# Kernel tuning notes

Hardware: AMD Instinct MI355X
Metric: run time of the kernel (lower is better)

The kernel has to match this reference:

```python
import jax, jax.numpy as jnp
import numpy as np

B, S, HID = 2, 2048, 2048
H = 16
Q_LORA, KV_LORA = 1536, 512
D_NOPE, D_ROPE, D_V = 128, 64, 128
D_QK = D_NOPE + D_ROPE  # 192
EPS = 1e-6


def rms_norm(x, w):
    var = jnp.mean(jnp.square(x), axis=-1, keepdims=True)
    return x * jax.lax.rsqrt(var + EPS) * w


def apply_rope(x, cos, sin):
    # x: [..., d] with interleaved (real, imag) pairs; cos/sin broadcastable to [..., d//2]
    xr = x[..., 0::2]
    xi = x[..., 1::2]
    or_ = xr * cos - xi * sin
    oi_ = xr * sin + xi * cos
    return jnp.stack([or_, oi_], axis=-1).reshape(x.shape)


def setup_inputs() -> dict:
    key = jax.random.key(0)
    ks = jax.random.split(key, 8)
    std = 0.02
    x = jax.random.normal(ks[0], (B, S, HID), dtype=jnp.float32)
    # rotary frequencies (real cos/sin pair per complex freq)
    inv_freq = 1.0 / (10000.0 ** (np.arange(0, D_ROPE, 2, dtype=np.float32) / D_ROPE))
    t = np.arange(S, dtype=np.float32)
    ang = np.outer(t, inv_freq)  # [S, D_ROPE//2]
    freqs_cis = jnp.asarray(np.stack([np.cos(ang), np.sin(ang)], axis=-1))  # [S, 32, 2]
    return {
        "x": x,
        "freqs_cis": freqs_cis,
        "wq_a": std * jax.random.normal(ks[1], (Q_LORA, HID), dtype=jnp.float32),
        "q_a_norm_w": jnp.ones((Q_LORA,), dtype=jnp.float32),
        "wq_b": std * jax.random.normal(ks[2], (H * D_QK, Q_LORA), dtype=jnp.float32),
        "wkv_a": std * jax.random.normal(ks[3], (KV_LORA + D_ROPE, HID), dtype=jnp.float32),
        "kv_norm_w": jnp.ones((KV_LORA,), dtype=jnp.float32),
        "wkv_b": std * jax.random.normal(ks[4], (H * (D_NOPE + D_V), KV_LORA), dtype=jnp.float32),
        "wo": std * jax.random.normal(ks[5], (HID, H * D_V), dtype=jnp.float32),
    }


def mla_forward(x, freqs_cis, wq_a, q_a_norm_w, wq_b, wkv_a, kv_norm_w, wkv_b, wo):
    cos = freqs_cis[..., 0]  # [S, D_ROPE//2]
    sin = freqs_cis[..., 1]
    # --- queries: low-rank down, RMSNorm, up ---
    q = rms_norm(x @ wq_a.T, q_a_norm_w) @ wq_b.T          # [B,S,H*D_QK]
    q = q.reshape(B, S, H, D_QK)
    q_nope, q_pe = q[..., :D_NOPE], q[..., D_NOPE:]
    q_pe = apply_rope(q_pe, cos[None, :, None, :], sin[None, :, None, :])
    q = jnp.concatenate([q_nope, q_pe], axis=-1)           # [B,S,H,D_QK]
    # --- kv latent + shared rope key ---
    kv_all = x @ wkv_a.T                                   # [B,S,KV_LORA+D_ROPE]
    kv_lat, k_pe = kv_all[..., :KV_LORA], kv_all[..., KV_LORA:]
    k_pe = apply_rope(k_pe, cos[None, :, :], sin[None, :, :])   # [B,S,D_ROPE]
    kv = rms_norm(kv_lat, kv_norm_w) @ wkv_b.T             # [B,S,H*(D_NOPE+D_V)]
    kv = kv.reshape(B, S, H, D_NOPE + D_V)
    k_nope, v = kv[..., :D_NOPE], kv[..., D_NOPE:]
    k = jnp.concatenate(
        [k_nope, jnp.broadcast_to(k_pe[:, :, None, :], (B, S, H, D_ROPE))], axis=-1
    )                                                      # [B,S,H,D_QK]
    # --- causal softmax attention ---
    scale = D_QK ** -0.5
    scores = jnp.einsum("bqhd,bkhd->bhqk", q, k) * scale   # [B,H,S,S]
    causal = jnp.tril(jnp.ones((S, S), dtype=bool))
    scores = jnp.where(causal, scores, jnp.finfo(scores.dtype).min)
    probs = jax.nn.softmax(scores, axis=-1)
    out = jnp.einsum("bhqk,bkhd->bqhd", probs, v)          # [B,S,H,D_V]
    return out.reshape(B, S, H * D_V) @ wo.T               # [B,S,HID]


def reference(x, freqs_cis, wq_a, q_a_norm_w, wq_b, wkv_a, kv_norm_w, wkv_b, wo):
    return mla_forward(x, freqs_cis, wq_a, q_a_norm_w, wq_b, wkv_a, kv_norm_w, wkv_b, wo)
```

## Files before the change

kernel.cpp:

```cpp
#include <hip/hip_runtime.h>

typedef __bf16 bf16_t;
typedef bf16_t bf16x8 __attribute__((ext_vector_type(8)));
typedef bf16_t bf16x4v __attribute__((ext_vector_type(4)));
typedef float f32x4 __attribute__((ext_vector_type(4)));

static constexpr float QSCALE = 0.07216878364870323f * 1.44269504088896341f;

#define AS1 __attribute__((address_space(1)))
#define AS3 __attribute__((address_space(3)))
__device__ __forceinline__ void g2lds16(const void* g, void* l) {
  __builtin_amdgcn_global_load_lds((const AS1 void*)g, (AS3 void*)l, 16, 0, 0);
}

__global__ void k_cast_bf16(const float* __restrict__ in, bf16_t* __restrict__ out, int n8) {
  int i = blockIdx.x * 256 + threadIdx.x;
  if (i >= n8) return;
  const float4* p = (const float4*)in + (size_t)i * 2;
  float4 a = p[0], b = p[1];
  bf16x8 o = {(bf16_t)a.x, (bf16_t)a.y, (bf16_t)a.z, (bf16_t)a.w,
              (bf16_t)b.x, (bf16_t)b.y, (bf16_t)b.z, (bf16_t)b.w};
  ((bf16x8*)out)[i] = o;
}

__global__ __launch_bounds__(256) void k_gemm(
    const bf16_t* __restrict__ A, const bf16_t* __restrict__ Bt,
    float* __restrict__ C, int M, int N, int K) {
  __shared__ __align__(16) bf16_t As[128][32];
  __shared__ __align__(16) bf16_t Bs[128][32];
  const int tid = threadIdx.x;
  const int lane = tid & 63, wid = tid >> 6;
  const int wr = wid >> 1, wc = wid & 1;
  const int lr = lane & 15, lk = lane >> 4;
  const int bm = blockIdx.y * 128, bn = blockIdx.x * 128;
  f32x4 acc[4][4] = {};
  const int srow = wid * 16 + (lane >> 2);
  const int scol = (lane & 3) * 8;
  const bf16_t* a0 = A + (size_t)(bm + srow) * K + scol;
  const bf16_t* a1 = A + (size_t)(bm + 64 + srow) * K + scol;
  const bf16_t* b0 = Bt + (size_t)(bn + srow) * K + scol;
  const bf16_t* b1 = Bt + (size_t)(bn + 64 + srow) * K + scol;
  bf16_t* lA0 = &As[wid * 16][0];
  bf16_t* lA1 = &As[64 + wid * 16][0];
  bf16_t* lB0 = &Bs[wid * 16][0];
  bf16_t* lB1 = &Bs[64 + wid * 16][0];
  for (int kt = 0; kt < K; kt += 32) {
    g2lds16(a0 + kt, lA0);
    g2lds16(a1 + kt, lA1);
    g2lds16(b0 + kt, lB0);
    g2lds16(b1 + kt, lB1);
    __syncthreads();
    bf16x8 af[4], bff[4];
#pragma unroll
    for (int i = 0; i < 4; i++)
      af[i] = *(const bf16x8*)(&As[wr * 64 + i * 16 + lr][lk * 8]);
#pragma unroll
    for (int j = 0; j < 4; j++)
      bff[j] = *(const bf16x8*)(&Bs[wc * 64 + j * 16 + lr][lk * 8]);
#pragma unroll
    for (int i = 0; i < 4; i++)
#pragma unroll
      for (int j = 0; j < 4; j++)
        acc[i][j] = __builtin_amdgcn_mfma_f32_16x16x32_bf16(af[i], bff[j], acc[i][j], 0, 0, 0);
    __syncthreads();
  }
  const int crow = bm + wr * 64 + lk * 4;
  const int ccol = bn + wc * 64 + lr;
#pragma unroll
  for (int i = 0; i < 4; i++)
#pragma unroll
    for (int j = 0; j < 4; j++) {
      int col = ccol + j * 16;
      if (col < N) {
#pragma unroll
        for (int r = 0; r < 4; r++)
          C[(size_t)(crow + i * 16 + r) * N + col] = acc[i][j][r];
      }
    }
}

__global__ __launch_bounds__(256) void k_rms_q(const float* __restrict__ in,
                                               const float* __restrict__ w,
                                               bf16_t* __restrict__ out) {
  int row = blockIdx.x;
  const float4* x4 = (const float4*)(in + (size_t)row * 1536);
  float ss = 0.f;
  for (int i = threadIdx.x; i < 384; i += 256) {
    float4 v = x4[i];
    ss += v.x * v.x + v.y * v.y + v.z * v.z + v.w * v.w;
  }
  for (int m = 32; m; m >>= 1) ss += __shfl_xor(ss, m);
  __shared__ float parts[4];
  if ((threadIdx.x & 63) == 0) parts[threadIdx.x >> 6] = ss;
  __syncthreads();
  float inv = rsqrtf((parts[0] + parts[1] + parts[2] + parts[3]) * (1.f / 1536.f) + 1e-6f);
  const float4* w4 = (const float4*)w;
  for (int i = threadIdx.x; i < 384; i += 256) {
    float4 v = x4[i];
    float4 ww = w4[i];
    bf16x4v o = {(bf16_t)(v.x * inv * ww.x), (bf16_t)(v.y * inv * ww.y),
                 (bf16_t)(v.z * inv * ww.z), (bf16_t)(v.w * inv * ww.w)};
    *(bf16x4v*)(out + (size_t)row * 1536 + i * 4) = o;
  }
}

__global__ __launch_bounds__(256) void k_kv_norm_rope(const float* __restrict__ kvall,
                                                      const float* __restrict__ w,
                                                      const float* __restrict__ freqs,
                                                      bf16_t* __restrict__ kvn,
                                                      bf16_t* __restrict__ Kf) {
  int row = blockIdx.x, tid = threadIdx.x;
  int b = row >> 11, s = row & 2047;
  const float* x = kvall + (size_t)row * 576;
  float ss = 0.f;
  float4 v = {0.f, 0.f, 0.f, 0.f};
  if (tid < 128) {
    v = ((const float4*)x)[tid];
    ss = v.x * v.x + v.y * v.y + v.z * v.z + v.w * v.w;
  }
  for (int m = 32; m; m >>= 1) ss += __shfl_xor(ss, m);
  __shared__ float parts[4];
  if ((tid & 63) == 0) parts[tid >> 6] = ss;
  __syncthreads();
  float inv = rsqrtf((parts[0] + parts[1] + parts[2] + parts[3]) * (1.f / 512.f) + 1e-6f);
  if (tid < 128) {
    float4 ww = ((const float4*)w)[tid];
    bf16x4v o = {(bf16_t)(v.x * inv * ww.x), (bf16_t)(v.y * inv * ww.y),
                 (bf16_t)(v.z * inv * ww.z), (bf16_t)(v.w * inv * ww.w)};
    *(bf16x4v*)(kvn + (size_t)row * 512 + tid * 4) = o;
  }
  if (tid < 32) {
    float xr = x[512 + 2 * tid], xi = x[513 + 2 * tid];
    float c = freqs[s * 64 + 2 * tid], sn = freqs[s * 64 + 2 * tid + 1];
    bf16_t o0 = (bf16_t)(xr * c - xi * sn);
    bf16_t o1 = (bf16_t)(xr * sn + xi * c);
#pragma unroll
    for (int h = 0; h < 16; h++) {
      size_t base = ((size_t)(b * 16 + h) * 2048 + s) * 192 + 128 + 2 * tid;
      Kf[base] = o0;
      Kf[base + 1] = o1;
    }
  }
}

__global__ __launch_bounds__(256) void k_q_rope(const float* __restrict__ q,
                                                const float* __restrict__ freqs,
                                                bf16_t* __restrict__ Q) {
  int row = blockIdx.x;
  int b = row >> 11, s = row & 2047;
  const float* src = q + (size_t)row * 3072;
  const float* fr = freqs + s * 64;
#pragma unroll
  for (int i = 0; i < 12; i++) {
    int idx = i * 256 + threadIdx.x;
    int h = idx / 192, d = idx - h * 192;
    float val;
    if (d < 128) {
      val = src[h * 192 + d];
    } else {
      int p = (d - 128) >> 1;
      float xr = src[h * 192 + 128 + 2 * p], xi = src[h * 192 + 129 + 2 * p];
      float c = fr[2 * p], sn = fr[2 * p + 1];
      val = ((d & 1) == 0) ? (xr * c - xi * sn) : (xr * sn + xi * c);
    }
    Q[((size_t)(b * 16 + h) * 2048 + s) * 192 + d] = (bf16_t)(val * QSCALE);
  }
}

__global__ __launch_bounds__(256) void k_split_kv(const float* __restrict__ kvfull,
                                                  bf16_t* __restrict__ Kf,
                                                  bf16_t* __restrict__ Vt) {
  __shared__ bf16_t vt_l[128][66];
  int s0 = blockIdx.x * 64;
  int h = blockIdx.y;
#pragma unroll 4
  for (int i = 0; i < 32; i++) {
    int idx = i * 256 + threadIdx.x;
    int r = idx >> 7, d = idx & 127;
    int row = s0 + r;
    int b = row >> 11, s = row & 2047;
    const float* src = kvfull + (size_t)row * 4096 + h * 256;
    float kn = src[d], vv = src[128 + d];
    Kf[((size_t)(b * 16 + h) * 2048 + s) * 192 + d] = (bf16_t)kn;
    vt_l[d][r] = (bf16_t)vv;
  }
  __syncthreads();
#pragma unroll 4
  for (int i = 0; i < 32; i++) {
    int idx = i * 256 + threadIdx.x;
    int d = idx >> 6, ss = idx & 63;
    int row = s0 + ss;
    int b = row >> 11, s = row & 2047;
    Vt[((size_t)(b * 16 + h) * 128 + d) * 2048 + s] = vt_l[d][ss];
  }
}

__global__ __launch_bounds__(256) void k_attn(const bf16_t* __restrict__ Q,
                                              const bf16_t* __restrict__ Kf,
                                              const bf16_t* __restrict__ Vt,
                                              bf16_t* __restrict__ O) {
  __shared__ __align__(16) bf16_t Ks[3][64][64];
  __shared__ __align__(16) bf16_t Vs[128][64];
  __shared__ __align__(16) bf16_t P[4][16][72];
  const int tid = threadIdx.x;
  const int lane = tid & 63, wid = tid >> 6;
  const int lr = lane & 15, lk = lane >> 4;
  const int qt = (int)gridDim.x - 1 - (int)blockIdx.x;
  const int qb = qt * 64;
  const int qbw = qb + wid * 16;
  const int bh = blockIdx.y;
  const int b = bh >> 4, h = bh & 15;
  const bf16_t* Qb = Q + (size_t)bh * 2048 * 192;
  const bf16_t* Kb = Kf + (size_t)bh * 2048 * 192;
  const bf16_t* Vb = Vt + (size_t)bh * 128 * 2048;
  bf16x8 bq[6];
#pragma unroll
  for (int f = 0; f < 6; f++)
    bq[f] = *(const bf16x8*)(Qb + (size_t)(qbw + lr) * 192 + f * 32 + lk * 8);
  f32x4 acc[8] = {};
  float m_s = -1e30f, l_s = 0.f;
  const int q_mine = qbw + lr;
  const int srowb = tid >> 3;
  const int sc8 = tid & 7;
  auto stage = [&](int k0) {
#pragma unroll
    for (int p = 0; p < 3; p++)
#pragma unroll
      for (int hh2 = 0; hh2 < 2; hh2++) {
        int row = hh2 * 32 + srowb;
        g2lds16(Kb + (size_t)(k0 + row) * 192 + p * 64 + ((sc8 ^ (row & 7)) * 8),
                &Ks[p][row][sc8 * 8]);
      }
#pragma unroll
    for (int j = 0; j < 4; j++) {
      int d = j * 32 + srowb;
      g2lds16(Vb + (size_t)d * 2048 + k0 + ((sc8 ^ (d & 7)) * 8), &Vs[d][sc8 * 8]);
    }
  };
  const int nkt = qt + 1;
  stage(0);
  for (int kt = 0; kt < nkt; kt++) {
    const int k0 = kt * 64;
    __syncthreads();
    f32x4 sc[4];
#pragma unroll
    for (int hh = 0; hh < 4; hh++) {
      f32x4 a = {};
      const int row = hh * 16 + lr;
      const int sw = (row & 7);
#pragma unroll
      for (int f = 0; f < 6; f++) {
        const int cc = (f & 1) * 4 + lk;
        bf16x8 ak = *(const bf16x8*)(&Ks[f >> 1][row][(cc ^ sw) * 8]);
        a = __builtin_amdgcn_mfma_f32_16x16x32_bf16(ak, bq[f], a, 0, 0, 0);
      }
      sc[hh] = a;
    }
    if (k0 + 63 > qbw) {
#pragma unroll
      for (int hh = 0; hh < 4; hh++) {
        int key = k0 + hh * 16 + lk * 4;
#pragma unroll
        for (int r = 0; r < 4; r++)
          if (key + r > q_mine) sc[hh][r] = -1e30f;
      }
    }
    float t0 = fmaxf(fmaxf(sc[0][0], sc[0][1]), fmaxf(sc[0][2], sc[0][3]));
    float t1 = fmaxf(fmaxf(sc[1][0], sc[1][1]), fmaxf(sc[1][2], sc[1][3]));
    float t2 = fmaxf(fmaxf(sc[2][0], sc[2][1]), fmaxf(sc[2][2], sc[2][3]));
    float t3 = fmaxf(fmaxf(sc[3][0], sc[3][1]), fmaxf(sc[3][2], sc[3][3]));
    float tmax = fmaxf(fmaxf(t0, t1), fmaxf(t2, t3));
    tmax = fmaxf(tmax, __shfl_xor(tmax, 16));
    tmax = fmaxf(tmax, __shfl_xor(tmax, 32));
    float mn = fmaxf(m_s, tmax);
    float alpha = exp2f(m_s - mn);
    m_s = mn;
    float sm = 0.f;
#pragma unroll
    for (int hh = 0; hh < 4; hh++) {
#pragma unroll
      for (int r = 0; r < 4; r++) {
        float p = exp2f(sc[hh][r] - mn);
        sc[hh][r] = p;
        sm += p;
      }
    }
    sm += __shfl_xor(sm, 16);
    sm += __shfl_xor(sm, 32);
    l_s = l_s * alpha + sm;
#pragma unroll
    for (int hh = 0; hh < 4; hh++) {
      bf16x4v pv = {(bf16_t)sc[hh][0], (bf16_t)sc[hh][1], (bf16_t)sc[hh][2], (bf16_t)sc[hh][3]};
      *(bf16x4v*)(&P[wid][lr][hh * 16 + lk * 4]) = pv;
    }
    float ab[4];
#pragma unroll
    for (int r = 0; r < 4; r++) ab[r] = __shfl(alpha, lk * 4 + r);
#pragma unroll
    for (int j = 0; j < 8; j++)
#pragma unroll
      for (int r = 0; r < 4; r++) acc[j][r] *= ab[r];
#pragma unroll
    for (int s2 = 0; s2 < 2; s2++) {
      bf16x8 pa = *(const bf16x8*)(&P[wid][lr][s2 * 32 + lk * 8]);
#pragma unroll
      for (int j = 0; j < 8; j++) {
        const int d = j * 16 + lr;
        const int cc = s2 * 4 + lk;
        bf16x8 bv = *(const bf16x8*)(&Vs[d][(cc ^ (d & 7)) * 8]);
        acc[j] = __builtin_amdgcn_mfma_f32_16x16x32_bf16(pa, bv, acc[j], 0, 0, 0);
      }
    }
    __syncthreads();
    if (kt + 1 < nkt) stage(k0 + 64);
  }
  float linv = 1.f / l_s;
  float lb[4];
#pragma unroll
  for (int r = 0; r < 4; r++) lb[r] = __shfl(linv, lk * 4 + r);
  size_t orow = (size_t)b * 2048 + qbw + lk * 4;
#pragma unroll
  for (int j = 0; j < 8; j++)
#pragma unroll
    for (int r = 0; r < 4; r++)
      O[(orow + r) * 2048 + h * 128 + j * 16 + lr] = (bf16_t)(acc[j][r] * lb[r]);
}

extern "C" void kernel_launch(void* const* d_in, const int* in_sizes, int n_in,
                              void* d_out, int out_size, void* d_ws, size_t ws_size,
                              hipStream_t stream) {
  const float* x = (const float*)d_in[0];
  const float* freqs = (const float*)d_in[1];
  const float* wq_a = (const float*)d_in[2];
  const float* q_norm_w = (const float*)d_in[3];
  const float* wq_b = (const float*)d_in[4];
  const float* wkv_a = (const float*)d_in[5];
  const float* kv_norm_w = (const float*)d_in[6];
  const float* wkv_b = (const float*)d_in[7];
  const float* wo = (const float*)d_in[8];
  float* out = (float*)d_out;
  char* ws = (char*)d_ws;

  float* f32scr = (float*)(ws);
  bf16_t* xbf = (bf16_t*)(ws + 67108864);
  bf16_t* wqab = (bf16_t*)(ws + 83886080);
  bf16_t* wqbb = (bf16_t*)(ws + 90177536);
  bf16_t* wkvab = (bf16_t*)(ws + 99614720);
  bf16_t* wkvbb = (bf16_t*)(ws + 101974016);
  bf16_t* wob = (bf16_t*)(ws + 106168320);
  bf16_t* qan = (bf16_t*)(ws + 114556928);
  bf16_t* kvn = (bf16_t*)(ws + 127139840);
  bf16_t* Qb = (bf16_t*)(ws + 131334144);
  bf16_t* Kb = (bf16_t*)(ws + 156499968);
  bf16_t* Vtb = (bf16_t*)(ws + 181665792);
  bf16_t* aob = (bf16_t*)(ws + 198443008);
  (void)in_sizes; (void)n_in; (void)out_size; (void)ws_size;

  auto cast = [&](const float* src, bf16_t* dst, int n) {
    int n8 = n / 8;
    k_cast_bf16<<<(n8 + 255) / 256, 256, 0, stream>>>(src, dst, n8);
  };
  cast(x, xbf, 8388608);
  cast(wq_a, wqab, 3145728);
  cast(wq_b, wqbb, 4718592);
  cast(wkv_a, wkvab, 1179648);
  cast(wkv_b, wkvbb, 2097152);
  cast(wo, wob, 4194304);

  k_gemm<<<dim3(5, 32), 256, 0, stream>>>(xbf, wkvab, f32scr, 4096, 576, 2048);
  k_kv_norm_rope<<<4096, 256, 0, stream>>>(f32scr, kv_norm_w, freqs, kvn, Kb);
  k_gemm<<<dim3(32, 32), 256, 0, stream>>>(kvn, wkvbb, f32scr, 4096, 4096, 512);
  k_split_kv<<<dim3(64, 16), 256, 0, stream>>>(f32scr, Kb, Vtb);
  k_gemm<<<dim3(12, 32), 256, 0, stream>>>(xbf, wqab, f32scr, 4096, 1536, 2048);
  k_rms_q<<<4096, 256, 0, stream>>>(f32scr, q_norm_w, qan);
  k_gemm<<<dim3(24, 32), 256, 0, stream>>>(qan, wqbb, f32scr, 4096, 3072, 1536);
  k_q_rope<<<4096, 256, 0, stream>>>(f32scr, freqs, Qb);
  k_attn<<<dim3(32, 32), 256, 0, stream>>>(Qb, Kb, Vtb, aob);
  k_gemm<<<dim3(16, 32), 256, 0, stream>>>(aob, wob, out, 4096, 2048, 2048);
}
```

Before: 582.8 us.

## Emit bf16 GEMM outputs, fuse Q rope into GEMM, widen attention blocks

GEMM becomes a template that writes bf16 intermediates instead of fp32, and in one mode applies RoPE, the softmax scale and the head-major scatter directly in the epilogue, which removes the separate q_rope kernel. The downstream norm and split kernels read bf16, halving their intermediate traffic. The attention kernel now uses 512-thread blocks covering 128 queries. It replaces async global-to-LDS staging with register prefetch plus commit, and adds a rotation swizzle on the P buffer. Causally dead tiles are skipped per wave. Rounding the pre-norm intermediates to bf16 adds extra error.

```diff
diff --git a/kernel.cpp b/kernel.cpp
--- a/kernel.cpp
+++ b/kernel.cpp
@@ -23,9 +23,10 @@
   ((bf16x8*)out)[i] = o;
 }
 
-__global__ __launch_bounds__(256) void k_gemm(
+template <int MODE>
+__global__ __launch_bounds__(256) void k_gemm_t(
     const bf16_t* __restrict__ A, const bf16_t* __restrict__ Bt,
-    float* __restrict__ C, int M, int N, int K) {
+    void* __restrict__ Cout, int M, int N, int K, const float* __restrict__ freqs) {
   __shared__ __align__(16) bf16_t As[128][32];
   __shared__ __align__(16) bf16_t Bs[128][32];
   const int tid = threadIdx.x;
@@ -72,51 +73,83 @@
     for (int j = 0; j < 4; j++) {
       int col = ccol + j * 16;
       if (col < N) {
-#pragma unroll
-        for (int r = 0; r < 4; r++)
-          C[(size_t)(crow + i * 16 + r) * N + col] = acc[i][j][r];
+        if constexpr (MODE == 0) {
+          float* C = (float*)Cout;
+#pragma unroll
+          for (int r = 0; r < 4; r++)
+            C[(size_t)(crow + i * 16 + r) * N + col] = acc[i][j][r];
+        } else if constexpr (MODE == 1) {
+          bf16_t* C = (bf16_t*)Cout;
+#pragma unroll
+          for (int r = 0; r < 4; r++)
+            C[(size_t)(crow + i * 16 + r) * N + col] = (bf16_t)acc[i][j][r];
+        } else {
+          bf16_t* Qd = (bf16_t*)Cout;
+          int hcol = col / 192;
+          int dmod = col - hcol * 192;
+#pragma unroll
+          for (int r = 0; r < 4; r++) {
+            int row = crow + i * 16 + r;
+            int bb = row >> 11, s = row & 2047;
+            float v = acc[i][j][r];
+            float partner = __shfl_xor(v, 1);
+            if (dmod >= 128) {
+              int p = (dmod - 128) >> 1;
+              int pbase = ((lr & 1) == 0) ? (dmod - 128) : (dmod - 129);
+              p = pbase >> 1;
+              float c = freqs[s * 64 + 2 * p];
+              float sn = freqs[s * 64 + 2 * p + 1];
+              v = ((lr & 1) == 0) ? (v * c - partner * sn) : (partner * sn + v * c);
+            }
+            Qd[((size_t)(bb * 16 + hcol) * 2048 + s) * 192 + dmod] = (bf16_t)(v * QSCALE);
+          }
+        }
       }
     }
 }
 
-__global__ __launch_bounds__(256) void k_rms_q(const float* __restrict__ in,
+__global__ __launch_bounds__(256) void k_rms_q(const bf16_t* __restrict__ in,
                                                const float* __restrict__ w,
                                                bf16_t* __restrict__ out) {
-  int row = blockIdx.x;
-  const float4* x4 = (const float4*)(in + (size_t)row * 1536);
+  int row = blockIdx.x, tid = threadIdx.x;
+  const bf16x8* x8 = (const bf16x8*)(in + (size_t)row * 1536);
   float ss = 0.f;
-  for (int i = threadIdx.x; i < 384; i += 256) {
-    float4 v = x4[i];
-    ss += v.x * v.x + v.y * v.y + v.z * v.z + v.w * v.w;
+  bf16x8 v = {};
+  if (tid < 192) {
+    v = x8[tid];
+#pragma unroll
+    for (int j = 0; j < 8; j++) { float f = (float)v[j]; ss += f * f; }
   }
   for (int m = 32; m; m >>= 1) ss += __shfl_xor(ss, m);
   __shared__ float parts[4];
-  if ((threadIdx.x & 63) == 0) parts[threadIdx.x >> 6] = ss;
+  if ((tid & 63) == 0) parts[tid >> 6] = ss;
   __syncthreads();
   float inv = rsqrtf((parts[0] + parts[1] + parts[2] + parts[3]) * (1.f / 1536.f) + 1e-6f);
-  const float4* w4 = (const float4*)w;
-  for (int i = threadIdx.x; i < 384; i += 256) {
-    float4 v = x4[i];
-    float4 ww = w4[i];
-    bf16x4v o = {(bf16_t)(v.x * inv * ww.x), (bf16_t)(v.y * inv * ww.y),
-                 (bf16_t)(v.z * inv * ww.z), (bf16_t)(v.w * inv * ww.w)};
-    *(bf16x4v*)(out + (size_t)row * 1536 + i * 4) = o;
-  }
-}
-
-__global__ __launch_bounds__(256) void k_kv_norm_rope(const float* __restrict__ kvall,
+  if (tid < 192) {
+    const float4* w4 = (const float4*)(w + tid * 8);
+    float4 w0 = w4[0], w1 = w4[1];
+    bf16x8 o = {(bf16_t)((float)v[0] * inv * w0.x), (bf16_t)((float)v[1] * inv * w0.y),
+                (bf16_t)((float)v[2] * inv * w0.z), (bf16_t)((float)v[3] * inv * w0.w),
+                (bf16_t)((float)v[4] * inv * w1.x), (bf16_t)((float)v[5] * inv * w1.y),
+                (bf16_t)((float)v[6] * inv * w1.z), (bf16_t)((float)v[7] * inv * w1.w)};
+    *(bf16x8*)(out + (size_t)row * 1536 + tid * 8) = o;
+  }
+}
+
+__global__ __launch_bounds__(256) void k_kv_norm_rope(const bf16_t* __restrict__ kvall,
                                                       const float* __restrict__ w,
                                                       const float* __restrict__ freqs,
                                                       bf16_t* __restrict__ kvn,
                                                       bf16_t* __restrict__ Kf) {
   int row = blockIdx.x, tid = threadIdx.x;
   int b = row >> 11, s = row & 2047;
-  const float* x = kvall + (size_t)row * 576;
+  const bf16_t* x = kvall + (size_t)row * 576;
   float ss = 0.f;
-  float4 v = {0.f, 0.f, 0.f, 0.f};
+  float vf[4] = {0.f, 0.f, 0.f, 0.f};
   if (tid < 128) {
-    v = ((const float4*)x)[tid];
-    ss = v.x * v.x + v.y * v.y + v.z * v.z + v.w * v.w;
+    bf16x4v v4 = *(const bf16x4v*)(x + tid * 4);
+#pragma unroll
+    for (int j = 0; j < 4; j++) { vf[j] = (float)v4[j]; ss += vf[j] * vf[j]; }
   }
   for (int m = 32; m; m >>= 1) ss += __shfl_xor(ss, m);
   __shared__ float parts[4];
@@ -125,12 +158,12 @@
   float inv = rsqrtf((parts[0] + parts[1] + parts[2] + parts[3]) * (1.f / 512.f) + 1e-6f);
   if (tid < 128) {
     float4 ww = ((const float4*)w)[tid];
-    bf16x4v o = {(bf16_t)(v.x * inv * ww.x), (bf16_t)(v.y * inv * ww.y),
-                 (bf16_t)(v.z * inv * ww.z), (bf16_t)(v.w * inv * ww.w)};
+    bf16x4v o = {(bf16_t)(vf[0] * inv * ww.x), (bf16_t)(vf[1] * inv * ww.y),
+                 (bf16_t)(vf[2] * inv * ww.z), (bf16_t)(vf[3] * inv * ww.w)};
     *(bf16x4v*)(kvn + (size_t)row * 512 + tid * 4) = o;
   }
   if (tid < 32) {
-    float xr = x[512 + 2 * tid], xi = x[513 + 2 * tid];
+    float xr = (float)x[512 + 2 * tid], xi = (float)x[513 + 2 * tid];
     float c = freqs[s * 64 + 2 * tid], sn = freqs[s * 64 + 2 * tid + 1];
     bf16_t o0 = (bf16_t)(xr * c - xi * sn);
     bf16_t o1 = (bf16_t)(xr * sn + xi * c);
@@ -143,31 +176,7 @@
   }
 }
 
-__global__ __launch_bounds__(256) void k_q_rope(const float* __restrict__ q,
-                                                const float* __restrict__ freqs,
-                                                bf16_t* __restrict__ Q) {
-  int row = blockIdx.x;
-  int b = row >> 11, s = row & 2047;
-  const float* src = q + (size_t)row * 3072;
-  const float* fr = freqs + s * 64;
-#pragma unroll
-  for (int i = 0; i < 12; i++) {
-    int idx = i * 256 + threadIdx.x;
-    int h = idx / 192, d = idx - h * 192;
-    float val;
-    if (d < 128) {
-      val = src[h * 192 + d];
-    } else {
-      int p = (d - 128) >> 1;
-      float xr = src[h * 192 + 128 + 2 * p], xi = src[h * 192 + 129 + 2 * p];
-      float c = fr[2 * p], sn = fr[2 * p + 1];
-      val = ((d & 1) == 0) ? (xr * c - xi * sn) : (xr * sn + xi * c);
-    }
-    Q[((size_t)(b * 16 + h) * 2048 + s) * 192 + d] = (bf16_t)(val * QSCALE);
-  }
-}
-
-__global__ __launch_bounds__(256) void k_split_kv(const float* __restrict__ kvfull,
+__global__ __launch_bounds__(256) void k_split_kv(const bf16_t* __restrict__ kvfull,
                                                   bf16_t* __restrict__ Kf,
                                                   bf16_t* __restrict__ Vt) {
   __shared__ bf16_t vt_l[128][66];
@@ -179,10 +188,9 @@
     int r = idx >> 7, d = idx & 127;
     int row = s0 + r;
     int b = row >> 11, s = row & 2047;
-    const float* src = kvfull + (size_t)row * 4096 + h * 256;
-    float kn = src[d], vv = src[128 + d];
-    Kf[((size_t)(b * 16 + h) * 2048 + s) * 192 + d] = (bf16_t)kn;
-    vt_l[d][r] = (bf16_t)vv;
+    const bf16_t* src = kvfull + (size_t)row * 4096 + h * 256;
+    Kf[((size_t)(b * 16 + h) * 2048 + s) * 192 + d] = src[d];
+    vt_l[d][r] = src[128 + d];
   }
   __syncthreads();
 #pragma unroll 4
@@ -195,124 +203,133 @@
   }
 }
 
-__global__ __launch_bounds__(256) void k_attn(const bf16_t* __restrict__ Q,
+__global__ __launch_bounds__(512) void k_attn(const bf16_t* __restrict__ Q,
                                               const bf16_t* __restrict__ Kf,
                                               const bf16_t* __restrict__ Vt,
                                               bf16_t* __restrict__ O) {
   __shared__ __align__(16) bf16_t Ks[3][64][64];
   __shared__ __align__(16) bf16_t Vs[128][64];
-  __shared__ __align__(16) bf16_t P[4][16][72];
+  __shared__ __align__(16) bf16_t P[8][16][72];
   const int tid = threadIdx.x;
   const int lane = tid & 63, wid = tid >> 6;
   const int lr = lane & 15, lk = lane >> 4;
   const int qt = (int)gridDim.x - 1 - (int)blockIdx.x;
-  const int qb = qt * 64;
+  const int qb = qt * 128;
   const int qbw = qb + wid * 16;
   const int bh = blockIdx.y;
   const int b = bh >> 4, h = bh & 15;
-  const bf16_t* Qb = Q + (size_t)bh * 2048 * 192;
+  const bf16_t* Qp = Q + (size_t)bh * 2048 * 192;
   const bf16_t* Kb = Kf + (size_t)bh * 2048 * 192;
   const bf16_t* Vb = Vt + (size_t)bh * 128 * 2048;
   bf16x8 bq[6];
 #pragma unroll
   for (int f = 0; f < 6; f++)
-    bq[f] = *(const bf16x8*)(Qb + (size_t)(qbw + lr) * 192 + f * 32 + lk * 8);
+    bq[f] = *(const bf16x8*)(Qp + (size_t)(qbw + lr) * 192 + f * 32 + lk * 8);
   f32x4 acc[8] = {};
   float m_s = -1e30f, l_s = 0.f;
   const int q_mine = qbw + lr;
-  const int srowb = tid >> 3;
-  const int sc8 = tid & 7;
-  auto stage = [&](int k0) {
-#pragma unroll
-    for (int p = 0; p < 3; p++)
-#pragma unroll
-      for (int hh2 = 0; hh2 < 2; hh2++) {
-        int row = hh2 * 32 + srowb;
-        g2lds16(Kb + (size_t)(k0 + row) * 192 + p * 64 + ((sc8 ^ (row & 7)) * 8),
-                &Ks[p][row][sc8 * 8]);
-      }
-#pragma unroll
-    for (int j = 0; j < 4; j++) {
-      int d = j * 32 + srowb;
-      g2lds16(Vb + (size_t)d * 2048 + k0 + ((sc8 ^ (d & 7)) * 8), &Vs[d][sc8 * 8]);
-    }
+  const int krow = tid >> 3;
+  const int kc8 = tid & 7;
+  const int vd1 = 64 + krow;
+  bf16x8 kr0, kr1, kr2, vr0, vr1;
+  auto issue = [&](int k0) {
+    const bf16_t* kp = Kb + (size_t)(k0 + krow) * 192 + kc8 * 8;
+    kr0 = *(const bf16x8*)(kp);
+    kr1 = *(const bf16x8*)(kp + 64);
+    kr2 = *(const bf16x8*)(kp + 128);
+    vr0 = *(const bf16x8*)(Vb + (size_t)krow * 2048 + k0 + kc8 * 8);
+    vr1 = *(const bf16x8*)(Vb + (size_t)vd1 * 2048 + k0 + kc8 * 8);
   };
-  const int nkt = qt + 1;
-  stage(0);
+  auto commit = [&]() {
+    *(bf16x8*)(&Ks[0][krow][((kc8 + krow) & 7) * 8]) = kr0;
+    *(bf16x8*)(&Ks[1][krow][((kc8 + krow) & 7) * 8]) = kr1;
+    *(bf16x8*)(&Ks[2][krow][((kc8 + krow) & 7) * 8]) = kr2;
+    *(bf16x8*)(&Vs[krow][((kc8 + krow) & 7) * 8]) = vr0;
+    *(bf16x8*)(&Vs[vd1][((kc8 + vd1) & 7) * 8]) = vr1;
+  };
+  const int nkt = qt * 2 + 2;
+  issue(0);
+  commit();
+  __syncthreads();
   for (int kt = 0; kt < nkt; kt++) {
     const int k0 = kt * 64;
-    __syncthreads();
-    f32x4 sc[4];
-#pragma unroll
-    for (int hh = 0; hh < 4; hh++) {
-      f32x4 a = {};
-      const int row = hh * 16 + lr;
-      const int sw = (row & 7);
-#pragma unroll
-      for (int f = 0; f < 6; f++) {
-        const int cc = (f & 1) * 4 + lk;
-        bf16x8 ak = *(const bf16x8*)(&Ks[f >> 1][row][(cc ^ sw) * 8]);
-        a = __builtin_amdgcn_mfma_f32_16x16x32_bf16(ak, bq[f], a, 0, 0, 0);
-      }
-      sc[hh] = a;
-    }
-    if (k0 + 63 > qbw) {
+    if (kt + 1 < nkt) issue(k0 + 64);
+    if (k0 <= qbw + 15) {
+      f32x4 sc[4];
 #pragma unroll
       for (int hh = 0; hh < 4; hh++) {
-        int key = k0 + hh * 16 + lk * 4;
-#pragma unroll
-        for (int r = 0; r < 4; r++)
-          if (key + r > q_mine) sc[hh][r] = -1e30f;
-      }
-    }
-    float t0 = fmaxf(fmaxf(sc[0][0], sc[0][1]), fmaxf(sc[0][2], sc[0][3]));
-    float t1 = fmaxf(fmaxf(sc[1][0], sc[1][1]), fmaxf(sc[1][2], sc[1][3]));
-    float t2 = fmaxf(fmaxf(sc[2][0], sc[2][1]), fmaxf(sc[2][2], sc[2][3]));
-    float t3 = fmaxf(fmaxf(sc[3][0], sc[3][1]), fmaxf(sc[3][2], sc[3][3]));
-    float tmax = fmaxf(fmaxf(t0, t1), fmaxf(t2, t3));
-    tmax = fmaxf(tmax, __shfl_xor(tmax, 16));
-    tmax = fmaxf(tmax, __shfl_xor(tmax, 32));
-    float mn = fmaxf(m_s, tmax);
-    float alpha = exp2f(m_s - mn);
-    m_s = mn;
-    float sm = 0.f;
-#pragma unroll
-    for (int hh = 0; hh < 4; hh++) {
-#pragma unroll
-      for (int r = 0; r < 4; r++) {
-        float p = exp2f(sc[hh][r] - mn);
-        sc[hh][r] = p;
-        sm += p;
-      }
-    }
-    sm += __shfl_xor(sm, 16);
-    sm += __shfl_xor(sm, 32);
-    l_s = l_s * alpha + sm;
-#pragma unroll
-    for (int hh = 0; hh < 4; hh++) {
-      bf16x4v pv = {(bf16_t)sc[hh][0], (bf16_t)sc[hh][1], (bf16_t)sc[hh][2], (bf16_t)sc[hh][3]};
-      *(bf16x4v*)(&P[wid][lr][hh * 16 + lk * 4]) = pv;
-    }
-    float ab[4];
-#pragma unroll
-    for (int r = 0; r < 4; r++) ab[r] = __shfl(alpha, lk * 4 + r);
-#pragma unroll
-    for (int j = 0; j < 8; j++)
-#pragma unroll
-      for (int r = 0; r < 4; r++) acc[j][r] *= ab[r];
-#pragma unroll
-    for (int s2 = 0; s2 < 2; s2++) {
-      bf16x8 pa = *(const bf16x8*)(&P[wid][lr][s2 * 32 + lk * 8]);
-#pragma unroll
-      for (int j = 0; j < 8; j++) {
-        const int d = j * 16 + lr;
-        const int cc = s2 * 4 + lk;
-        bf16x8 bv = *(const bf16x8*)(&Vs[d][(cc ^ (d & 7)) * 8]);
-        acc[j] = __builtin_amdgcn_mfma_f32_16x16x32_bf16(pa, bv, acc[j], 0, 0, 0);
+        f32x4 a = {};
+        const int row = hh * 16 + lr;
+#pragma unroll
+        for (int f = 0; f < 6; f++) {
+          const int cc = (f & 1) * 4 + lk;
+          bf16x8 ak = *(const bf16x8*)(&Ks[f >> 1][row][((cc + row) & 7) * 8]);
+          a = __builtin_amdgcn_mfma_f32_16x16x32_bf16(ak, bq[f], a, 0, 0, 0);
+        }
+        sc[hh] = a;
+      }
+      if (k0 + 63 > qbw) {
+#pragma unroll
+        for (int hh = 0; hh < 4; hh++) {
+          int key = k0 + hh * 16 + lk * 4;
+#pragma unroll
+          for (int r = 0; r < 4; r++)
+            if (key + r > q_mine) sc[hh][r] = -1e30f;
+        }
+      }
+      float t0 = fmaxf(fmaxf(sc[0][0], sc[0][1]), fmaxf(sc[0][2], sc[0][3]));
+      float t1 = fmaxf(fmaxf(sc[1][0], sc[1][1]), fmaxf(sc[1][2], sc[1][3]));
+      float t2 = fmaxf(fmaxf(sc[2][0], sc[2][1]), fmaxf(sc[2][2], sc[2][3]));
+      float t3 = fmaxf(fmaxf(sc[3][0], sc[3][1]), fmaxf(sc[3][2], sc[3][3]));
+      float tmax = fmaxf(fmaxf(t0, t1), fmaxf(t2, t3));
+      tmax = fmaxf(tmax, __shfl_xor(tmax, 16));
+      tmax = fmaxf(tmax, __shfl_xor(tmax, 32));
+      float mn = fmaxf(m_s, tmax);
+      float alpha = exp2f(m_s - mn);
+      m_s = mn;
+      float sm = 0.f;
+#pragma unroll
+      for (int hh = 0; hh < 4; hh++) {
+#pragma unroll
+        for (int r = 0; r < 4; r++) {
+          float p = exp2f(sc[hh][r] - mn);
+          sc[hh][r] = p;
+          sm += p;
+        }
+      }
+      sm += __shfl_xor(sm, 16);
+      sm += __shfl_xor(sm, 32);
+      l_s = l_s * alpha + sm;
+#pragma unroll
+      for (int hh = 0; hh < 4; hh++) {
+        int c8 = hh * 2 + (lk >> 1);
+        int coff = ((c8 + lr) & 7) * 8 + (lk & 1) * 4;
+        bf16x4v pv = {(bf16_t)sc[hh][0], (bf16_t)sc[hh][1], (bf16_t)sc[hh][2], (bf16_t)sc[hh][3]};
+        *(bf16x4v*)(&P[wid][lr][coff]) = pv;
+      }
+      float ab[4];
+#pragma unroll
+      for (int r = 0; r < 4; r++) ab[r] = __shfl(alpha, lk * 4 + r);
+#pragma unroll
+      for (int j = 0; j < 8; j++)
+#pragma unroll
+        for (int r = 0; r < 4; r++) acc[j][r] *= ab[r];
+#pragma unroll
+      for (int s2 = 0; s2 < 2; s2++) {
+        bf16x8 pa = *(const bf16x8*)(&P[wid][lr][((s2 * 4 + lk + lr) & 7) * 8]);
+#pragma unroll
+        for (int j = 0; j < 8; j++) {
+          const int d = j * 16 + lr;
+          bf16x8 bv = *(const bf16x8*)(&Vs[d][((s2 * 4 + lk + d) & 7) * 8]);
+          acc[j] = __builtin_amdgcn_mfma_f32_16x16x32_bf16(pa, bv, acc[j], 0, 0, 0);
+        }
       }
     }
     __syncthreads();
-    if (kt + 1 < nkt) stage(k0 + 64);
+    if (kt + 1 < nkt) {
+      commit();
+      __syncthreads();
+    }
   }
   float linv = 1.f / l_s;
   float lb[4];
@@ -341,7 +358,9 @@
   float* out = (float*)d_out;
   char* ws = (char*)d_ws;
 
-  float* f32scr = (float*)(ws);
+  bf16_t* kvallb = (bf16_t*)(ws);
+  bf16_t* kvfullb = (bf16_t*)(ws + 8388608);
+  bf16_t* qab = (bf16_t*)(ws + 50331648);
   bf16_t* xbf = (bf16_t*)(ws + 67108864);
   bf16_t* wqab = (bf16_t*)(ws + 83886080);
   bf16_t* wqbb = (bf16_t*)(ws + 90177536);
@@ -367,14 +386,13 @@
   cast(wkv_b, wkvbb, 2097152);
   cast(wo, wob, 4194304);
 
-  k_gemm<<<dim3(5, 32), 256, 0, stream>>>(xbf, wkvab, f32scr, 4096, 576, 2048);
-  k_kv_norm_rope<<<4096, 256, 0, stream>>>(f32scr, kv_norm_w, freqs, kvn, Kb);
-  k_gemm<<<dim3(32, 32), 256, 0, stream>>>(kvn, wkvbb, f32scr, 4096, 4096, 512);
-  k_split_kv<<<dim3(64, 16), 256, 0, stream>>>(f32scr, Kb, Vtb);
-  k_gemm<<<dim3(12, 32), 256, 0, stream>>>(xbf, wqab, f32scr, 4096, 1536, 2048);
-  k_rms_q<<<4096, 256, 0, stream>>>(f32scr, q_norm_w, qan);
-  k_gemm<<<dim3(24, 32), 256, 0, stream>>>(qan, wqbb, f32scr, 4096, 3072, 1536);
-  k_q_rope<<<4096, 256, 0, stream>>>(f32scr, freqs, Qb);
-  k_attn<<<dim3(32, 32), 256, 0, stream>>>(Qb, Kb, Vtb, aob);
-  k_gemm<<<dim3(16, 32), 256, 0, stream>>>(aob, wob, out, 4096, 2048, 2048);
-}
+  k_gemm_t<1><<<dim3(5, 32), 256, 0, stream>>>(xbf, wkvab, kvallb, 4096, 576, 2048, nullptr);
+  k_kv_norm_rope<<<4096, 256, 0, stream>>>(kvallb, kv_norm_w, freqs, kvn, Kb);
+  k_gemm_t<1><<<dim3(32, 32), 256, 0, stream>>>(kvn, wkvbb, kvfullb, 4096, 4096, 512, nullptr);
+  k_split_kv<<<dim3(64, 16), 256, 0, stream>>>(kvfullb, Kb, Vtb);
+  k_gemm_t<1><<<dim3(12, 32), 256, 0, stream>>>(xbf, wqab, qab, 4096, 1536, 2048, nullptr);
+  k_rms_q<<<4096, 256, 0, stream>>>(qab, q_norm_w, qan);
+  k_gemm_t<2><<<dim3(24, 32), 256, 0, stream>>>(qan, wqbb, Qb, 4096, 3072, 1536, freqs);
+  k_attn<<<dim3(16, 32), 512, 0, stream>>>(Qb, Kb, Vtb, aob);
+  k_gemm_t<0><<<dim3(16, 32), 256, 0, stream>>>(aob, wob, out, 4096, 2048, 2048, nullptr);
+}
```

New measurement: 579.8 us. About the same (-0.5%).
